# Optimization experiments

Measured on AMD Instinct MI355X. Metric: run time of the kernel, lower is better.

Reference implementation:

```python
import jax, jax.numpy as jnp
import numpy as np

B, T, D, H = 2, 2048, 1024, 16
DK = D // H


def setup_inputs() -> dict:
    key = jax.random.key(0)
    ks = jax.random.split(key, 9)
    x = jax.random.normal(ks[0], (B, T, D), dtype=jnp.float32)
    # causal mask, broadcastable to [B, H, T, T]; positions with 0 are masked
    mask = jnp.tril(jnp.ones((T, T), dtype=jnp.int32))[None, None]
    s = 1.0 / np.sqrt(D)
    Wq = jax.random.normal(ks[1], (D, D), dtype=jnp.float32) * s
    Wk = jax.random.normal(ks[2], (D, D), dtype=jnp.float32) * s
    Wv = jax.random.normal(ks[3], (D, D), dtype=jnp.float32) * s
    Wo = jax.random.normal(ks[4], (D, D), dtype=jnp.float32) * s
    bq = jnp.zeros((D,), jnp.float32)
    bk = jnp.zeros((D,), jnp.float32)
    bv = jnp.zeros((D,), jnp.float32)
    bo = jnp.zeros((D,), jnp.float32)
    return {"x": x, "mask": mask, "Wq": Wq, "bq": bq, "Wk": Wk, "bk": bk,
            "Wv": Wv, "bv": bv, "Wo": Wo, "bo": bo}


def _split_heads(t):
    # [B, T, D] -> [B, H, T, DK]
    return t.reshape(B, T, H, DK).transpose(0, 2, 1, 3)


def reference(x, mask, Wq, bq, Wk, bk, Wv, bv, Wo, bo):
    Q = _split_heads(x @ Wq.T + bq)
    K = _split_heads(x @ Wk.T + bk)
    V = _split_heads(x @ Wv.T + bv)
    scores = jnp.einsum('bhqd,bhkd->bhqk', Q, K) / jnp.sqrt(jnp.float32(DK))
    scores = jnp.where(mask == 0, jnp.float32(-1e9), scores)
    attn = jax.nn.softmax(scores, axis=-1)  # dropout p=0 -> identity
    out = jnp.einsum('bhqk,bhkd->bhqd', attn, V)
    out = out.transpose(0, 2, 1, 3).reshape(B, T, D)
    out = out @ Wo.T + bo
    return (out, attn)
```

## Files before the change

kernel.cpp:

```cpp
#include <hip/hip_runtime.h>
#include <hip/hip_bf16.h>
#include <cstdint>


typedef __attribute__((ext_vector_type(8))) short bf16x8;
typedef __attribute__((ext_vector_type(4))) float f32x4;

#define MFMA(a,b,c) __builtin_amdgcn_mfma_f32_16x16x32_bf16((a),(b),(c),0,0,0)

static __device__ __forceinline__ short f2bf(float f) {
  __hip_bfloat16 h = __float2bfloat16(f);
  return (short)__builtin_bit_cast(ushort, h);
}

static __device__ __forceinline__ bf16x8 cvt8(const float* p) {
  float4 v0 = *(const float4*)p;
  float4 v1 = *(const float4*)(p + 4);
  bf16x8 r;
  r[0] = f2bf(v0.x); r[1] = f2bf(v0.y); r[2] = f2bf(v0.z); r[3] = f2bf(v0.w);
  r[4] = f2bf(v1.x); r[5] = f2bf(v1.y); r[6] = f2bf(v1.z); r[7] = f2bf(v1.w);
  return r;
}

__global__ __launch_bounds__(256)
void cvt_x(const float* __restrict__ x, ushort* __restrict__ xbf)
{
  const size_t i = ((size_t)blockIdx.x * 256 + threadIdx.x) * 8;
  const bf16x8 v = cvt8(x + i);
  *(bf16x8*)&xbf[i] = v;
}

__global__ __launch_bounds__(256)
void qkv_zeros(const ushort* __restrict__ Xbf,
               const float* __restrict__ Wq, const float* __restrict__ Wk,
               const float* __restrict__ Wv,
               const float* __restrict__ bq, const float* __restrict__ bk,
               const float* __restrict__ bv,
               ushort* __restrict__ Qw, ushort* __restrict__ Kw, ushort* __restrict__ Vt,
               float* __restrict__ attn)
{
  __shared__ __align__(16) ushort As[128 * 32];
  __shared__ __align__(16) ushort Bs[128 * 32];
  const int tid  = threadIdx.x;
  const int lane = tid & 63;
  const int wid  = tid >> 6;

  if (blockIdx.x >= 768) {
    const int zi = blockIdx.x - 768;
    const int qtile = zi % 31;
    const int bh = zi / 31;
    const int zstart = (qtile + 1) * 64;
    const int zlen = 2048 - zstart;
    float* base = attn + ((size_t)bh * 2048 + qtile * 64) * 2048;
    const f32x4 z = (f32x4){0.f, 0.f, 0.f, 0.f};
#pragma unroll
    for (int rr = 0; rr < 16; ++rr) {
      float* rowp = base + (size_t)(wid * 16 + rr) * 2048 + zstart;
      for (int c = lane * 4; c < zlen; c += 256)
        __builtin_nontemporal_store(z, (f32x4*)(rowp + c));
    }
    return;
  }

  const int wr = wid >> 1, wc = wid & 1;
  const int g = lane >> 4, c16 = lane & 15;
  const int i0 = (blockIdx.x & 31) * 128;
  const int j0 = (blockIdx.x >> 5) * 128;

  const int widx = j0 >> 10;
  const int jj0  = j0 & 1023;
  const float* W    = (widx == 0) ? Wq : ((widx == 1) ? Wk : Wv);
  const float* bias = (widx == 0) ? bq : ((widx == 1) ? bk : bv);

  const int arow = tid >> 2;
  const int acol = (tid & 3) * 8;
  const ushort* a0p = Xbf + (size_t)(i0 + arow) * 1024 + acol;
  const ushort* a1p = a0p + (size_t)64 * 1024;
  const float*  b0p = W + (size_t)(jj0 + arow) * 1024 + acol;
  const float*  b1p = b0p + (size_t)64 * 1024;

  f32x4 acc[4][4];
#pragma unroll
  for (int mi = 0; mi < 4; ++mi)
#pragma unroll
    for (int ni = 0; ni < 4; ++ni) acc[mi][ni] = (f32x4){0.f, 0.f, 0.f, 0.f};

  for (int k0 = 0; k0 < 1024; k0 += 32) {
    const bf16x8 va0 = *(const bf16x8*)(a0p + k0);
    const bf16x8 va1 = *(const bf16x8*)(a1p + k0);
    const bf16x8 vb0 = cvt8(b0p + k0);
    const bf16x8 vb1 = cvt8(b1p + k0);
    __syncthreads();
    *(bf16x8*)&As[tid * 8]        = va0;
    *(bf16x8*)&As[2048 + tid * 8] = va1;
    *(bf16x8*)&Bs[tid * 8]        = vb0;
    *(bf16x8*)&Bs[2048 + tid * 8] = vb1;
    __syncthreads();
    bf16x8 af[4], bfv[4];
#pragma unroll
    for (int mi = 0; mi < 4; ++mi)
      af[mi] = *(const bf16x8*)&As[(wr * 64 + mi * 16 + c16) * 32 + g * 8];
#pragma unroll
    for (int ni = 0; ni < 4; ++ni)
      bfv[ni] = *(const bf16x8*)&Bs[(wc * 64 + ni * 16 + c16) * 32 + g * 8];
#pragma unroll
    for (int mi = 0; mi < 4; ++mi)
#pragma unroll
      for (int ni = 0; ni < 4; ++ni)
        acc[mi][ni] = MFMA(af[mi], bfv[ni], acc[mi][ni]);
  }

  float bv4[4];
#pragma unroll
  for (int ni = 0; ni < 4; ++ni) bv4[ni] = bias[jj0 + wc * 64 + ni * 16 + c16];

  if (widx < 2) {
    ushort* OP = (widx == 0) ? Qw : Kw;
#pragma unroll
    for (int mi = 0; mi < 4; ++mi) {
      const int ib = i0 + wr * 64 + mi * 16 + g * 4;
      const int b = ib >> 11, t = ib & 2047;
#pragma unroll
      for (int ni = 0; ni < 4; ++ni) {
        const int jj = jj0 + wc * 64 + ni * 16 + c16;
        const int h = jj >> 6, dk = jj & 63;
        const size_t base = ((size_t)(b * 16 + h) * 2048 + t) * 64 + dk;
#pragma unroll
        for (int r = 0; r < 4; ++r)
          OP[base + (size_t)r * 64] = (ushort)f2bf(acc[mi][ni][r] + bv4[ni]);
      }
    }
  } else {
#pragma unroll
    for (int mi = 0; mi < 4; ++mi) {
      const int ib = i0 + wr * 64 + mi * 16 + g * 4;
      const int b = ib >> 11, t = ib & 2047;
#pragma unroll
      for (int ni = 0; ni < 4; ++ni) {
        const int jj = jj0 + wc * 64 + ni * 16 + c16;
        ushort4 pk;
        pk.x = (ushort)f2bf(acc[mi][ni][0] + bv4[ni]);
        pk.y = (ushort)f2bf(acc[mi][ni][1] + bv4[ni]);
        pk.z = (ushort)f2bf(acc[mi][ni][2] + bv4[ni]);
        pk.w = (ushort)f2bf(acc[mi][ni][3] + bv4[ni]);
        *(ushort4*)&Vt[((size_t)b * 1024 + jj) * 2048 + t] = pk;
      }
    }
  }
}

__global__ __launch_bounds__(256)
void attn_stats(const ushort* __restrict__ Qw, const ushort* __restrict__ Kw,
                const ushort* __restrict__ Vt, ushort* __restrict__ ctx,
                float* __restrict__ Linv)
{
  __shared__ __align__(16) ushort Ks[2][64][68];
  __shared__ __align__(16) ushort Vs[2][64][68];
  __shared__ __align__(16) ushort Plds[4][16][68];
  const int tid = threadIdx.x, lane = tid & 63, wid = tid >> 6;
  const int g = lane >> 4, c16 = lane & 15;
  const int pr = blockIdx.x & 15;
  const int bh = blockIdx.x >> 4;
  const int b = bh >> 4, h = bh & 15;

  const ushort* kbase = Kw + (size_t)bh * (2048 * 64);
  const ushort* vbase = Vt + ((size_t)b * 1024 + h * 64) * 2048;

  const int sr = tid >> 2;
  const int sc = (tid & 3) * 16;
  const ushort* kst = kbase + (size_t)sr * 64 + sc;
  const ushort* vst = vbase + (size_t)sr * 2048 + sc;

  int cur = 0;

#pragma unroll
  for (int part = 0; part < 2; ++part) {
    const int qtile = part ? (31 - pr) : pr;
    const int qt = qtile * 64 + wid * 16;
    const int q = qt + c16;
    const int nch = qtile + 1;

    const ushort* qp = Qw + ((size_t)bh * 2048 + q) * 64 + g * 8;
    const bf16x8 qf0 = *(const bf16x8*)qp;
    const bf16x8 qf1 = *(const bf16x8*)(qp + 32);

    f32x4 o[4];
#pragma unroll
    for (int dt = 0; dt < 4; ++dt) o[dt] = (f32x4){0.f, 0.f, 0.f, 0.f};
    float lsum = 0.f;

    {
      const bf16x8 k0 = *(const bf16x8*)kst;
      const bf16x8 k1 = *(const bf16x8*)(kst + 8);
      const bf16x8 v0 = *(const bf16x8*)vst;
      const bf16x8 v1 = *(const bf16x8*)(vst + 8);
      __syncthreads();
      *(bf16x8*)&Ks[cur][sr][sc]     = k0;
      *(bf16x8*)&Ks[cur][sr][sc + 8] = k1;
      *(bf16x8*)&Vs[cur][sr][sc]     = v0;
      *(bf16x8*)&Vs[cur][sr][sc + 8] = v1;
    }

    for (int c = 0; c < nch; ++c) {
      bf16x8 k0, k1, v0, v1;
      const bool pf = (c + 1 < nch);
      if (pf) {
        const int kt1 = (c + 1) * 64;
        k0 = *(const bf16x8*)(kst + (size_t)kt1 * 64);
        k1 = *(const bf16x8*)(kst + (size_t)kt1 * 64 + 8);
        v0 = *(const bf16x8*)(vst + kt1);
        v1 = *(const bf16x8*)(vst + kt1 + 8);
      }
      __syncthreads();

      const int kt = c * 64;
      f32x4 sv[4];
#pragma unroll
      for (int s = 0; s < 4; ++s) {
        const bf16x8 kf0 = *(const bf16x8*)&Ks[cur][s * 16 + c16][g * 8];
        const bf16x8 kf1 = *(const bf16x8*)&Ks[cur][s * 16 + c16][32 + g * 8];
        f32x4 t0 = (f32x4){0.f, 0.f, 0.f, 0.f};
        t0 = MFMA(kf0, qf0, t0);
        t0 = MFMA(kf1, qf1, t0);
        sv[s] = t0;
      }

      if (c + 1 == nch) {
#pragma unroll
        for (int s = 0; s < 4; ++s) {
          short pk[4];
#pragma unroll
          for (int r = 0; r < 4; ++r) {
            const int k = kt + s * 16 + g * 4 + r;
            const float p = (k > q) ? 0.f : __expf(sv[s][r] * 0.125f - 20.f);
            lsum += p;
            pk[r] = f2bf(p);
          }
          *(short4*)&Plds[wid][c16][s * 16 + g * 4] = *(short4*)pk;
        }
      } else {
#pragma unroll
        for (int s = 0; s < 4; ++s) {
          short pk[4];
#pragma unroll
          for (int r = 0; r < 4; ++r) {
            const float p = __expf(sv[s][r] * 0.125f - 20.f);
            lsum += p;
            pk[r] = f2bf(p);
          }
          *(short4*)&Plds[wid][c16][s * 16 + g * 4] = *(short4*)pk;
        }
      }

      {
        const bf16x8 pa0 = *(const bf16x8*)&Plds[wid][c16][g * 8];
#pragma unroll
        for (int dt = 0; dt < 4; ++dt) {
          const bf16x8 vf = *(const bf16x8*)&Vs[cur][dt * 16 + c16][g * 8];
          o[dt] = MFMA(pa0, vf, o[dt]);
        }
        const bf16x8 pa1 = *(const bf16x8*)&Plds[wid][c16][32 + g * 8];
#pragma unroll
        for (int dt = 0; dt < 4; ++dt) {
          const bf16x8 vf = *(const bf16x8*)&Vs[cur][dt * 16 + c16][32 + g * 8];
          o[dt] = MFMA(pa1, vf, o[dt]);
        }
      }

      if (pf) {
        *(bf16x8*)&Ks[cur ^ 1][sr][sc]     = k0;
        *(bf16x8*)&Ks[cur ^ 1][sr][sc + 8] = k1;
        *(bf16x8*)&Vs[cur ^ 1][sr][sc]     = v0;
        *(bf16x8*)&Vs[cur ^ 1][sr][sc + 8] = v1;
        cur ^= 1;
      }
    }

    lsum += __shfl_xor(lsum, 16);
    lsum += __shfl_xor(lsum, 32);
    const float linv = 1.f / lsum;
    if (g == 0) Linv[(size_t)bh * 2048 + q] = linv;

#pragma unroll
    for (int r = 0; r < 4; ++r) {
      const float lr = __shfl(linv, g * 4 + r);
#pragma unroll
      for (int dt = 0; dt < 4; ++dt)
        ctx[((size_t)(b * 2048 + qt + g * 4 + r)) * 1024 + h * 64 + dt * 16 + c16] =
            (ushort)f2bf(o[dt][r] * lr);
    }
  }
}

__global__ __launch_bounds__(256)
void out_tiles(const ushort* __restrict__ Qw, const ushort* __restrict__ Kw,
               const float* __restrict__ Linv, float* __restrict__ attn,
               const ushort* __restrict__ ctx, const float* __restrict__ Wo,
               const float* __restrict__ bo, float* __restrict__ out)
{
  __shared__ __align__(16) ushort As[128 * 32];
  __shared__ __align__(16) ushort Bs[128 * 32];
  const int tid = threadIdx.x, lane = tid & 63, wid = tid >> 6;
  const int g = lane >> 4, c16 = lane & 15;

  if (blockIdx.x >= 256) {
    const int ti = blockIdx.x - 256;
    const int bx = ti % 132;
    const int bh = ti / 132;
    const int n = bx * 4 + wid;
    int qtile = (int)((sqrtf(8.f * n + 1.f) - 1.f) * 0.5f);
    while ((qtile + 1) * (qtile + 2) / 2 <= n) ++qtile;
    while (qtile * (qtile + 1) / 2 > n) --qtile;
    const int ktile = n - qtile * (qtile + 1) / 2;
    const int qt0 = qtile * 64, kt0 = ktile * 64;
    float* abase = attn + ((size_t)bh * 2048) * 2048;

    const ushort* qbase = Qw + ((size_t)bh * 2048 + qt0) * 64;
    const ushort* kbase = Kw + ((size_t)bh * 2048 + kt0) * 64;
    bf16x8 qf0[4], qf1[4];
    float lv[4];
#pragma unroll
    for (int sq = 0; sq < 4; ++sq) {
      const ushort* qp = qbase + (size_t)(sq * 16 + c16) * 64 + g * 8;
      qf0[sq] = *(const bf16x8*)qp;
      qf1[sq] = *(const bf16x8*)(qp + 32);
      lv[sq] = Linv[(size_t)bh * 2048 + qt0 + sq * 16 + c16];
    }

    if (ktile < qtile) {
#pragma unroll
      for (int sk = 0; sk < 4; ++sk) {
        const ushort* kp = kbase + (size_t)(sk * 16 + c16) * 64 + g * 8;
        const bf16x8 kf0 = *(const bf16x8*)kp;
        const bf16x8 kf1 = *(const bf16x8*)(kp + 32);
#pragma unroll
        for (int sq = 0; sq < 4; ++sq) {
          f32x4 t = (f32x4){0.f, 0.f, 0.f, 0.f};
          t = MFMA(kf0, qf0[sq], t);
          t = MFMA(kf1, qf1[sq], t);
          const int qq = qt0 + sq * 16 + c16;
          f32x4 st;
#pragma unroll
          for (int r = 0; r < 4; ++r)
            st[r] = __expf(t[r] * 0.125f - 20.f) * lv[sq];
          __builtin_nontemporal_store(st,
              (f32x4*)(abase + (size_t)qq * 2048 + kt0 + sk * 16 + g * 4));
        }
      }
    } else {
#pragma unroll
      for (int sk = 0; sk < 4; ++sk) {
        const ushort* kp = kbase + (size_t)(sk * 16 + c16) * 64 + g * 8;
        const bf16x8 kf0 = *(const bf16x8*)kp;
        const bf16x8 kf1 = *(const bf16x8*)(kp + 32);
#pragma unroll
        for (int sq = 0; sq < 4; ++sq) {
          f32x4 t = (f32x4){0.f, 0.f, 0.f, 0.f};
          t = MFMA(kf0, qf0[sq], t);
          t = MFMA(kf1, qf1[sq], t);
          const int qq = qt0 + sq * 16 + c16;
          f32x4 st;
#pragma unroll
          for (int r = 0; r < 4; ++r) {
            const int kk = kt0 + sk * 16 + g * 4 + r;
            st[r] = (kk > qq) ? 0.f : __expf(t[r] * 0.125f - 20.f) * lv[sq];
          }
          __builtin_nontemporal_store(st,
              (f32x4*)(abase + (size_t)qq * 2048 + kt0 + sk * 16 + g * 4));
        }
      }
    }
    return;
  }

  const int j = blockIdx.x;
  const int wr = wid >> 1, wc = wid & 1;
  const int i0 = (j & 31) * 128;
  const int j0 = (j >> 5) * 128;

  const int arow = tid >> 2;
  const int acol = (tid & 3) * 8;
  const ushort* a0p = ctx + (size_t)(i0 + arow) * 1024 + acol;
  const ushort* a1p = a0p + (size_t)64 * 1024;
  const float*  b0p = Wo + (size_t)(j0 + arow) * 1024 + acol;
  const float*  b1p = b0p + (size_t)64 * 1024;

  f32x4 acc[4][4];
#pragma unroll
  for (int mi = 0; mi < 4; ++mi)
#pragma unroll
    for (int ni = 0; ni < 4; ++ni) acc[mi][ni] = (f32x4){0.f, 0.f, 0.f, 0.f};

  for (int k0 = 0; k0 < 1024; k0 += 32) {
    const bf16x8 va0 = *(const bf16x8*)(a0p + k0);
    const bf16x8 va1 = *(const bf16x8*)(a1p + k0);
    const bf16x8 vb0 = cvt8(b0p + k0);
    const bf16x8 vb1 = cvt8(b1p + k0);
    __syncthreads();
    *(bf16x8*)&As[tid * 8]        = va0;
    *(bf16x8*)&As[2048 + tid * 8] = va1;
    *(bf16x8*)&Bs[tid * 8]        = vb0;
    *(bf16x8*)&Bs[2048 + tid * 8] = vb1;
    __syncthreads();
    bf16x8 af[4], bfv[4];
#pragma unroll
    for (int mi = 0; mi < 4; ++mi)
      af[mi] = *(const bf16x8*)&As[(wr * 64 + mi * 16 + c16) * 32 + g * 8];
#pragma unroll
    for (int ni = 0; ni < 4; ++ni)
      bfv[ni] = *(const bf16x8*)&Bs[(wc * 64 + ni * 16 + c16) * 32 + g * 8];
#pragma unroll
    for (int mi = 0; mi < 4; ++mi)
#pragma unroll
      for (int ni = 0; ni < 4; ++ni)
        acc[mi][ni] = MFMA(af[mi], bfv[ni], acc[mi][ni]);
  }

  float bv4[4];
#pragma unroll
  for (int ni = 0; ni < 4; ++ni) bv4[ni] = bo[j0 + wc * 64 + ni * 16 + c16];

#pragma unroll
  for (int mi = 0; mi < 4; ++mi) {
    const int ib = i0 + wr * 64 + mi * 16 + g * 4;
#pragma unroll
    for (int ni = 0; ni < 4; ++ni) {
      const int jj = j0 + wc * 64 + ni * 16 + c16;
#pragma unroll
      for (int r = 0; r < 4; ++r)
        out[(size_t)(ib + r) * 1024 + jj] = acc[mi][ni][r] + bv4[ni];
    }
  }
}

extern "C" void kernel_launch(void* const* d_in, const int* in_sizes, int n_in,
                              void* d_out, int out_size, void* d_ws, size_t ws_size,
                              hipStream_t stream)
{
  const float* x  = (const float*)d_in[0];
  const float* Wq = (const float*)d_in[2];
  const float* bq = (const float*)d_in[3];
  const float* Wk = (const float*)d_in[4];
  const float* bk = (const float*)d_in[5];
  const float* Wv = (const float*)d_in[6];
  const float* bv = (const float*)d_in[7];
  const float* Wo = (const float*)d_in[8];
  const float* bo = (const float*)d_in[9];

  if (ws_size < (size_t)33816576) return;

  float* out  = (float*)d_out;
  float* attn = out + (size_t)4194304;

  ushort* ws   = (ushort*)d_ws;
  ushort* Qw   = ws;
  ushort* Kw   = Qw + (size_t)4194304;
  ushort* Vtw  = Kw + (size_t)4194304;
  ushort* ctx  = Vtw + (size_t)4194304;
  float*  Linv = (float*)(ctx + (size_t)4194304);

  cvt_x<<<dim3(2048), 256, 0, stream>>>(x, ctx);
  qkv_zeros<<<dim3(1760), 256, 0, stream>>>(ctx, Wq, Wk, Wv, bq, bk, bv,
                                            Qw, Kw, Vtw, attn);
  attn_stats<<<dim3(512), 256, 0, stream>>>(Qw, Kw, Vtw, ctx, Linv);
  out_tiles<<<dim3(4480), 256, 0, stream>>>(Qw, Kw, Linv, attn, ctx, Wo, bo, out);
}
```

Before: 232.9 us.

## Pre-convert QKV weights to bf16 in scratch and widen attention blocks

The Wq/Wk/Wv matrices are now converted to bf16 once, in the initial conversion kernel. They are stored temporarily in a region of the attention-probability output that is overwritten later. The QKV GEMM then loads bf16 weights directly, so it no longer re-reads fp32 weights and re-converts them in every tile. The attention-stats kernel moves to 512-thread blocks that cover 128-query tiles on a 2D grid, with single 16-byte K/V staging loads per thread. The causal mask check is now applied in every chunk instead of a separate last-chunk path. Reusing the output buffer as scratch depends on the later kernels' write order, and halving the block count may reduce occupancy balance.

```diff
diff --git a/kernel.cpp b/kernel.cpp
--- a/kernel.cpp
+++ b/kernel.cpp
@@ -22,18 +22,32 @@
   return r;
 }
 
+static __device__ __forceinline__ size_t wbf_off(int J, int k) {
+  return (size_t)((J >> 9) * 2048 + 1536 + (J & 511)) * 4096 + k;
+}
+
 __global__ __launch_bounds__(256)
-void cvt_x(const float* __restrict__ x, ushort* __restrict__ xbf)
+void cvt_xw(const float* __restrict__ x,
+            const float* __restrict__ Wq, const float* __restrict__ Wk,
+            const float* __restrict__ Wv,
+            ushort* __restrict__ xbf, ushort* __restrict__ attnU)
 {
-  const size_t i = ((size_t)blockIdx.x * 256 + threadIdx.x) * 8;
-  const bf16x8 v = cvt8(x + i);
-  *(bf16x8*)&xbf[i] = v;
+  if (blockIdx.x < 2048) {
+    const size_t i = ((size_t)blockIdx.x * 256 + threadIdx.x) * 8;
+    *(bf16x8*)&xbf[i] = cvt8(x + i);
+  } else {
+    const size_t e = ((size_t)(blockIdx.x - 2048) * 256 + threadIdx.x) * 8;
+    const int J = (int)(e >> 10);
+    const int k = (int)(e & 1023);
+    const int widx = J >> 10, j = J & 1023;
+    const float* W = (widx == 0) ? Wq : ((widx == 1) ? Wk : Wv);
+    const bf16x8 v = cvt8(W + (size_t)j * 1024 + k);
+    *(bf16x8*)&attnU[wbf_off(J, k)] = v;
+  }
 }
 
 __global__ __launch_bounds__(256)
-void qkv_zeros(const ushort* __restrict__ Xbf,
-               const float* __restrict__ Wq, const float* __restrict__ Wk,
-               const float* __restrict__ Wv,
+void qkv_zeros(const ushort* __restrict__ Xbf, const ushort* __restrict__ WbfU,
                const float* __restrict__ bq, const float* __restrict__ bk,
                const float* __restrict__ bv,
                ushort* __restrict__ Qw, ushort* __restrict__ Kw, ushort* __restrict__ Vt,
@@ -69,15 +83,15 @@
 
   const int widx = j0 >> 10;
   const int jj0  = j0 & 1023;
-  const float* W    = (widx == 0) ? Wq : ((widx == 1) ? Wk : Wv);
   const float* bias = (widx == 0) ? bq : ((widx == 1) ? bk : bv);
 
   const int arow = tid >> 2;
   const int acol = (tid & 3) * 8;
   const ushort* a0p = Xbf + (size_t)(i0 + arow) * 1024 + acol;
   const ushort* a1p = a0p + (size_t)64 * 1024;
-  const float*  b0p = W + (size_t)(jj0 + arow) * 1024 + acol;
-  const float*  b1p = b0p + (size_t)64 * 1024;
+  const int J0 = widx * 1024 + jj0 + arow;
+  const ushort* b0p = WbfU + wbf_off(J0, acol);
+  const ushort* b1p = WbfU + wbf_off(J0 + 64, acol);
 
   f32x4 acc[4][4];
 #pragma unroll
@@ -88,8 +102,8 @@
   for (int k0 = 0; k0 < 1024; k0 += 32) {
     const bf16x8 va0 = *(const bf16x8*)(a0p + k0);
     const bf16x8 va1 = *(const bf16x8*)(a1p + k0);
-    const bf16x8 vb0 = cvt8(b0p + k0);
-    const bf16x8 vb1 = cvt8(b1p + k0);
+    const bf16x8 vb0 = *(const bf16x8*)(b0p + k0);
+    const bf16x8 vb1 = *(const bf16x8*)(b1p + k0);
     __syncthreads();
     *(bf16x8*)&As[tid * 8]        = va0;
     *(bf16x8*)&As[2048 + tid * 8] = va1;
@@ -149,25 +163,25 @@
   }
 }
 
-__global__ __launch_bounds__(256)
+__global__ __launch_bounds__(512)
 void attn_stats(const ushort* __restrict__ Qw, const ushort* __restrict__ Kw,
                 const ushort* __restrict__ Vt, ushort* __restrict__ ctx,
                 float* __restrict__ Linv)
 {
   __shared__ __align__(16) ushort Ks[2][64][68];
   __shared__ __align__(16) ushort Vs[2][64][68];
-  __shared__ __align__(16) ushort Plds[4][16][68];
+  __shared__ __align__(16) ushort Plds[8][16][68];
   const int tid = threadIdx.x, lane = tid & 63, wid = tid >> 6;
   const int g = lane >> 4, c16 = lane & 15;
-  const int pr = blockIdx.x & 15;
-  const int bh = blockIdx.x >> 4;
+  const int pr = blockIdx.x;
+  const int bh = blockIdx.y;
   const int b = bh >> 4, h = bh & 15;
 
   const ushort* kbase = Kw + (size_t)bh * (2048 * 64);
   const ushort* vbase = Vt + ((size_t)b * 1024 + h * 64) * 2048;
 
-  const int sr = tid >> 2;
-  const int sc = (tid & 3) * 16;
+  const int sr = tid >> 3;
+  const int sc = (tid & 7) * 8;
   const ushort* kst = kbase + (size_t)sr * 64 + sc;
   const ushort* vst = vbase + (size_t)sr * 2048 + sc;
 
@@ -175,10 +189,10 @@
 
 #pragma unroll
   for (int part = 0; part < 2; ++part) {
-    const int qtile = part ? (31 - pr) : pr;
-    const int qt = qtile * 64 + wid * 16;
+    const int jt = part ? (15 - pr) : pr;
+    const int qt = jt * 128 + wid * 16;
     const int q = qt + c16;
-    const int nch = qtile + 1;
+    const int nch = 2 * jt + 2;
 
     const ushort* qp = Qw + ((size_t)bh * 2048 + q) * 64 + g * 8;
     const bf16x8 qf0 = *(const bf16x8*)qp;
@@ -191,25 +205,19 @@
 
     {
       const bf16x8 k0 = *(const bf16x8*)kst;
-      const bf16x8 k1 = *(const bf16x8*)(kst + 8);
       const bf16x8 v0 = *(const bf16x8*)vst;
-      const bf16x8 v1 = *(const bf16x8*)(vst + 8);
       __syncthreads();
-      *(bf16x8*)&Ks[cur][sr][sc]     = k0;
-      *(bf16x8*)&Ks[cur][sr][sc + 8] = k1;
-      *(bf16x8*)&Vs[cur][sr][sc]     = v0;
-      *(bf16x8*)&Vs[cur][sr][sc + 8] = v1;
+      *(bf16x8*)&Ks[cur][sr][sc] = k0;
+      *(bf16x8*)&Vs[cur][sr][sc] = v0;
     }
 
     for (int c = 0; c < nch; ++c) {
-      bf16x8 k0, k1, v0, v1;
+      bf16x8 kn, vn;
       const bool pf = (c + 1 < nch);
       if (pf) {
         const int kt1 = (c + 1) * 64;
-        k0 = *(const bf16x8*)(kst + (size_t)kt1 * 64);
-        k1 = *(const bf16x8*)(kst + (size_t)kt1 * 64 + 8);
-        v0 = *(const bf16x8*)(vst + kt1);
-        v1 = *(const bf16x8*)(vst + kt1 + 8);
+        kn = *(const bf16x8*)(kst + (size_t)kt1 * 64);
+        vn = *(const bf16x8*)(vst + kt1);
       }
       __syncthreads();
 
@@ -225,31 +233,17 @@
         sv[s] = t0;
       }
 
-      if (c + 1 == nch) {
-#pragma unroll
-        for (int s = 0; s < 4; ++s) {
-          short pk[4];
-#pragma unroll
-          for (int r = 0; r < 4; ++r) {
-            const int k = kt + s * 16 + g * 4 + r;
-            const float p = (k > q) ? 0.f : __expf(sv[s][r] * 0.125f - 20.f);
-            lsum += p;
-            pk[r] = f2bf(p);
-          }
-          *(short4*)&Plds[wid][c16][s * 16 + g * 4] = *(short4*)pk;
+#pragma unroll
+      for (int s = 0; s < 4; ++s) {
+        short pk[4];
+#pragma unroll
+        for (int r = 0; r < 4; ++r) {
+          const int k = kt + s * 16 + g * 4 + r;
+          const float p = (k > q) ? 0.f : __expf(sv[s][r] * 0.125f - 20.f);
+          lsum += p;
+          pk[r] = f2bf(p);
         }
-      } else {
-#pragma unroll
-        for (int s = 0; s < 4; ++s) {
-          short pk[4];
-#pragma unroll
-          for (int r = 0; r < 4; ++r) {
-            const float p = __expf(sv[s][r] * 0.125f - 20.f);
-            lsum += p;
-            pk[r] = f2bf(p);
-          }
-          *(short4*)&Plds[wid][c16][s * 16 + g * 4] = *(short4*)pk;
-        }
+        *(short4*)&Plds[wid][c16][s * 16 + g * 4] = *(short4*)pk;
       }
 
       {
@@ -268,10 +262,8 @@
       }
 
       if (pf) {
-        *(bf16x8*)&Ks[cur ^ 1][sr][sc]     = k0;
-        *(bf16x8*)&Ks[cur ^ 1][sr][sc + 8] = k1;
-        *(bf16x8*)&Vs[cur ^ 1][sr][sc]     = v0;
-        *(bf16x8*)&Vs[cur ^ 1][sr][sc + 8] = v1;
+        *(bf16x8*)&Ks[cur ^ 1][sr][sc] = kn;
+        *(bf16x8*)&Vs[cur ^ 1][sr][sc] = vn;
         cur ^= 1;
       }
     }
@@ -451,6 +443,7 @@
 
   float* out  = (float*)d_out;
   float* attn = out + (size_t)4194304;
+  ushort* attnU = (ushort*)attn;
 
   ushort* ws   = (ushort*)d_ws;
   ushort* Qw   = ws;
@@ -459,9 +452,9 @@
   ushort* ctx  = Vtw + (size_t)4194304;
   float*  Linv = (float*)(ctx + (size_t)4194304);
 
-  cvt_x<<<dim3(2048), 256, 0, stream>>>(x, ctx);
-  qkv_zeros<<<dim3(1760), 256, 0, stream>>>(ctx, Wq, Wk, Wv, bq, bk, bv,
+  cvt_xw<<<dim3(3584), 256, 0, stream>>>(x, Wq, Wk, Wv, ctx, attnU);
+  qkv_zeros<<<dim3(1760), 256, 0, stream>>>(ctx, attnU, bq, bk, bv,
                                             Qw, Kw, Vtw, attn);
-  attn_stats<<<dim3(512), 256, 0, stream>>>(Qw, Kw, Vtw, ctx, Linv);
+  attn_stats<<<dim3(8, 32), 512, 0, stream>>>(Qw, Kw, Vtw, ctx, Linv);
   out_tiles<<<dim3(4480), 256, 0, stream>>>(Qw, Kw, Linv, attn, ctx, Wo, bo, out);
 }
```

Measured after the change: 231.7 us. About the same (-0.5%).
